# Kernel optimization log

Measured on AMD Instinct MI355X. Metric: run time of the kernel, lower is better.

## Reference

```python
import jax, jax.numpy as jnp
import numpy as np

N = 16384       # number of points (single graph; batch all zeros)
DIN = 3         # input_dim
DOUT = 3        # output_dim
H = 16          # hidden_dim
K = 16          # k nearest neighbors
L = 4           # n_edgeconvs


def setup_inputs() -> dict:
    key = jax.random.key(0)
    ks = jax.random.split(key, 6)
    def w(k, shape, fan_in):
        return jax.random.normal(k, shape, jnp.float32) / np.float32(np.sqrt(fan_in))
    return {
        "x":     jax.random.normal(ks[0], (N, DIN), jnp.float32),
        "emb_W": w(ks[1], (DIN, H), DIN),
        "emb_b": jnp.zeros((H,), jnp.float32),
        "ec_W1": w(ks[2], (L, 2 * H, H), 2 * H),
        "ec_b1": jnp.zeros((L, H), jnp.float32),
        "ec_W2": w(ks[3], (L, H, H), H),
        "ec_b2": jnp.zeros((L, H), jnp.float32),
        "out_W": w(ks[4], (L * H, DOUT), L * H),
        "out_b": jnp.zeros((DOUT,), jnp.float32),
    }


def knn_idx(x, k):
    """Indices [N, k] of k nearest neighbors (no self-loops), like torch_cluster.knn_graph."""
    x = jax.lax.stop_gradient(x)  # graph construction is non-differentiable
    sq = jnp.sum(x * x, axis=-1)
    d = sq[:, None] + sq[None, :] - 2.0 * (x @ x.T)  # [N, N] squared distances
    n = x.shape[0]
    d = d.at[jnp.arange(n), jnp.arange(n)].set(jnp.inf)  # exclude self
    _, idx = jax.lax.top_k(-d, k)
    return idx  # idx[i] = k nearest neighbors j of center i


def edgeconv(x, idx, W1, b1, W2, b2):
    """EdgeConv with aggr='mean': mean_j MLP([x_i, x_j - x_i])."""
    nbr = x[idx]                                      # [N, K, H] gather
    ctr = jnp.broadcast_to(x[:, None, :], nbr.shape)  # [N, K, H]
    feat = jnp.concatenate([ctr, nbr - ctr], axis=-1) # [N, K, 2H]
    msg = jax.nn.relu(feat @ W1 + b1) @ W2 + b2       # [N, K, H]
    return jnp.mean(msg, axis=1)                      # exact k-regular scatter-mean


def reference(x, emb_W, emb_b, ec_W1, ec_b1, ec_W2, ec_b2, out_W, out_b):
    h = jax.nn.relu(x @ emb_W + emb_b)  # embedding
    outs = []
    for l in range(L):  # small fixed layer loop
        idx = knn_idx(h, K)  # kNN graph rebuilt on current features each layer
        h = edgeconv(h, idx, ec_W1[l], ec_b1[l], ec_W2[l], ec_b2[l])
        outs.append(h)
    return jnp.concatenate(outs, axis=-1) @ out_W + out_b  # [N, DOUT]
```

## Files before the change

### kernel.cpp

```cpp
#include <hip/hip_runtime.h>
#include <hip/hip_bf16.h>

#define GN 16384
#define GH 16
#define GK 16
#define GL 4
#define HPS 20

#define RPB 32
#define NTHR 1024
#define CAP 160
#define BSTR 161
#define SSTR 264
#define TILE_C 256
#define TILE_F (TILE_C*HPS)
#define LDS_TILE (2*RPB*BSTR + 2*RPB)
#define LDS_TOT  (LDS_TILE + TILE_F)

#define INFF __builtin_inff()

#define OFF_H     0
#define OFF_IDX   (5*GN*HPS)
#define OFF_FLAGS (OFF_IDX + GN*GK)
#define OFF_XF    (OFF_FLAGS + GN)
#define OFF_EMBW  (OFF_XF + GN*3)
#define OFF_EMBB  (OFF_EMBW + 3*GH)
#define OFF_W1    (OFF_EMBB + GH)
#define OFF_B1    (OFF_W1 + GL*2*GH*GH)
#define OFF_B2_   (OFF_B1 + GL*GH)
#define OFF_W2    OFF_B2_
#define OFF_B2    (OFF_W2 + GL*GH*GH)
#define OFF_OW    (OFF_B2 + GL*GH)
#define OFF_OB    (OFF_OW + GL*GH*3)
#define OFF_DFLAG (OFF_OB + 4)

__global__ void detect_kernel(const unsigned short* __restrict__ raw,
                              int* __restrict__ flag)
{
    if (threadIdx.x == 0 && blockIdx.x == 0) {
        int cnt = 0;
        for (int i = 0; i < 64; ++i) {
            unsigned int bits = ((unsigned int)raw[2*i]) << 16;
            float v = __uint_as_float(bits);
            float a = fabsf(v);
            if (a > 1e-4f && a < 50.f) ++cnt;
        }
        *flag = (cnt >= 32) ? 1 : 0;
    }
}

__global__ void convert_kernel(const void* __restrict__ src,
                               float* __restrict__ dst, int n,
                               const int* __restrict__ flag)
{
    int i = blockIdx.x * 256 + threadIdx.x;
    if (i >= n) return;
    if (*flag)
        dst[i] = __bfloat162float(((const __hip_bfloat16*)src)[i]);
    else
        dst[i] = ((const float*)src)[i];
}

__device__ __forceinline__ float distt(const float hi[16], float sqi,
                                       const float* __restrict__ hj)
{
    float4 A = *(const float4*)(hj + 0);
    float4 B = *(const float4*)(hj + 4);
    float4 C = *(const float4*)(hj + 8);
    float4 D = *(const float4*)(hj + 12);
    float sqj = hj[16];
    float d0 = hi[0]*A.x;
    float d1 = hi[1]*A.y;
    d0 = fmaf(hi[2],  A.z, d0);  d1 = fmaf(hi[3],  A.w, d1);
    d0 = fmaf(hi[4],  B.x, d0);  d1 = fmaf(hi[5],  B.y, d1);
    d0 = fmaf(hi[6],  B.z, d0);  d1 = fmaf(hi[7],  B.w, d1);
    d0 = fmaf(hi[8],  C.x, d0);  d1 = fmaf(hi[9],  C.y, d1);
    d0 = fmaf(hi[10], C.z, d0);  d1 = fmaf(hi[11], C.w, d1);
    d0 = fmaf(hi[12], D.x, d0);  d1 = fmaf(hi[13], D.y, d1);
    d0 = fmaf(hi[14], D.z, d0);  d1 = fmaf(hi[15], D.w, d1);
    return fmaf(-2.f, d0 + d1, sqi + sqj);
}

#define LOAD_HI(ptr)                                                        \
    float hi[16]; float sqi;                                                \
    {                                                                       \
        const float* _hr = (ptr);                                           \
        float4 A = *(const float4*)(_hr + 0);                               \
        float4 B = *(const float4*)(_hr + 4);                               \
        float4 C = *(const float4*)(_hr + 8);                               \
        float4 D = *(const float4*)(_hr + 12);                              \
        hi[0]=A.x; hi[1]=A.y; hi[2]=A.z; hi[3]=A.w;                         \
        hi[4]=B.x; hi[5]=B.y; hi[6]=B.z; hi[7]=B.w;                         \
        hi[8]=C.x; hi[9]=C.y; hi[10]=C.z; hi[11]=C.w;                       \
        hi[12]=D.x; hi[13]=D.y; hi[14]=D.z; hi[15]=D.w;                     \
        sqi = _hr[16];                                                      \
    }

__global__ __launch_bounds__(256) void embed_kernel(
    const float* __restrict__ xf, const float* __restrict__ W,
    const float* __restrict__ b, float* __restrict__ h0)
{
    int i = blockIdx.x * 256 + threadIdx.x;
    float x0 = xf[i*3+0], x1 = xf[i*3+1], x2 = xf[i*3+2];
    float* orow = h0 + i * HPS;
    float sq = 0.f;
#pragma unroll
    for (int c = 0; c < GH; ++c) {
        float t = b[c];
        t = fmaf(x0, W[0*GH+c], t);
        t = fmaf(x1, W[1*GH+c], t);
        t = fmaf(x2, W[2*GH+c], t);
        t = fmaxf(t, 0.f);
        orow[c] = t;
        sq = fmaf(t, t, sq);
    }
    orow[16] = sq;
}

__global__ __launch_bounds__(NTHR, 4) void knn3_kernel(
    const float* __restrict__ hp, int* __restrict__ idxout,
    int* __restrict__ flags)
{
    __shared__ float lds[LDS_TOT];
    float*    bufd = lds;
    int*      bufj = (int*)(lds + RPB*BSTR);
    unsigned* cnt  = (unsigned*)(lds + 2*RPB*BSTR);
    float*    tau  = lds + 2*RPB*BSTR + RPB;
    float*    tile = lds + LDS_TILE;

    const int tid  = threadIdx.x;
    const int r    = tid & 31;
    const int slot = tid >> 5;
    const int row  = blockIdx.x * RPB + r;

    LOAD_HI(hp + row * HPS);

#define STAGE(tb, sh)                                                        \
    for (int v = tid; v < TILE_C*5; v += NTHR) {                             \
        int c = v / 5;                                                       \
        int f = v - c*5;                                                     \
        ((float4*)tile)[v] = ((const float4*)hp)[((tb) + (c << (sh)))*5 + f];\
    }

    float t8[8];
#pragma unroll
    for (int s = 0; s < 8; ++s) t8[s] = INFF;
    float mx = INFF; int mxs = 0;
    for (int k = 0; k < GN/1024; ++k) {
        __syncthreads();
        STAGE(k*1024, 2);
        __syncthreads();
        const float* sb = tile + (slot*8)*HPS;
#pragma unroll 2
        for (int t = 0; t < 8; ++t) {
            int j = k*1024 + ((slot*8 + t) << 2);
            float d = distt(hi, sqi, sb + t*HPS);
            if (j == row) d = INFF;
            if (d < mx) {
#pragma unroll
                for (int q = 0; q < 8; ++q) { bool cs = (q == mxs); t8[q] = cs ? d : t8[q]; }
                mx = t8[0]; mxs = 0;
#pragma unroll
                for (int q = 1; q < 8; ++q) { bool cs = (t8[q] >= mx); mx = cs ? t8[q] : mx; mxs = cs ? q : mxs; }
            }
        }
    }
    __syncthreads();
    *(float4*)(lds + r*SSTR + slot*8)     = make_float4(t8[0], t8[1], t8[2], t8[3]);
    *(float4*)(lds + r*SSTR + slot*8 + 4) = make_float4(t8[4], t8[5], t8[6], t8[7]);
    __syncthreads();

    const int mr = tid >> 5, g = tid & 31;
    float s8[8];
    {
        float4 u0 = *(const float4*)(lds + mr*SSTR + g*8);
        float4 u1 = *(const float4*)(lds + mr*SSTR + g*8 + 4);
        s8[0]=u0.x; s8[1]=u0.y; s8[2]=u0.z; s8[3]=u0.w;
        s8[4]=u1.x; s8[5]=u1.y; s8[6]=u1.z; s8[7]=u1.w;
    }
    float tval = INFF;
#pragma unroll
    for (int k = 0; k < 16; ++k) {
        float md = s8[0]; int ms = 0;
#pragma unroll
        for (int q = 1; q < 8; ++q) { bool cs = (s8[q] < md); md = cs ? s8[q] : md; ms = cs ? q : ms; }
        float rv = md; int rl = g;
#pragma unroll
        for (int m = 1; m <= 16; m <<= 1) {
            float ov = __shfl_xor(rv, m, 32);
            int   ol = __shfl_xor(rl, m, 32);
            bool cs = (ov < rv) || (ov == rv && ol < rl);
            rv = cs ? ov : rv; rl = cs ? ol : rl;
        }
        if (rl == g) {
#pragma unroll
            for (int q = 0; q < 8; ++q) if (q == ms) s8[q] = INFF;
        }
        tval = rv;
    }
    if (g == 0) tau[mr] = tval;
    if (tid < RPB) cnt[tid] = 0;
    __syncthreads();

    const float taur = tau[r];
    const int rowoff = r * BSTR;
    for (int k = 0; k < GN/TILE_C; ++k) {
        __syncthreads();
        STAGE(k*TILE_C, 0);
        __syncthreads();
        const float* sb = tile + (slot*8)*HPS;
#pragma unroll 2
        for (int t = 0; t < 8; ++t) {
            int j = k*TILE_C + slot*8 + t;
            float d = distt(hi, sqi, sb + t*HPS);
            if (j == row) d = INFF;
            if (d <= taur) {
                unsigned pos = atomicAdd(&cnt[r], 1u);
                if (pos < CAP) { bufd[rowoff + pos] = d; bufj[rowoff + pos] = j; }
            }
        }
    }
    __syncthreads();

    const unsigned c   = cnt[mr];
    const unsigned lim = c < CAP ? c : CAP;
    float sd[5]; int sj[5];
#pragma unroll
    for (int e = 0; e < 5; ++e) {
        unsigned p = (unsigned)g + 32u*e;
        bool v = p < lim;
        sd[e] = v ? bufd[mr*BSTR + p] : INFF;
        sj[e] = v ? bufj[mr*BSTR + p] : 0x7fffffff;
    }
    const int rowg = blockIdx.x * RPB + mr;
#pragma unroll
    for (int k = 0; k < GK; ++k) {
        float md = sd[0]; int mj = sj[0]; int ms = 0;
#pragma unroll
        for (int e = 1; e < 5; ++e) {
            bool cs = (sd[e] < md) || (sd[e] == md && sj[e] < mj);
            md = cs ? sd[e] : md; mj = cs ? sj[e] : mj; ms = cs ? e : ms;
        }
        float rd = md; int rj = mj;
#pragma unroll
        for (int m = 1; m <= 16; m <<= 1) {
            float od = __shfl_xor(rd, m, 32);
            int   oj = __shfl_xor(rj, m, 32);
            bool cs = (od < rd) || (od == rd && oj < rj);
            rd = cs ? od : rd; rj = cs ? oj : rj;
        }
        if (g == 0) idxout[rowg*GK + k] = rj;
        if (rd == md && rj == mj) {
#pragma unroll
            for (int e = 0; e < 5; ++e) if (e == ms) { sd[e] = INFF; sj[e] = 0x7fffffff; }
        }
    }
    if (g == 0) flags[rowg] = (c > CAP || c < 16u) ? 1 : 0;
#undef STAGE
}

__global__ __launch_bounds__(64) void rescue_kernel(
    const float* __restrict__ hp, const int* __restrict__ flags,
    int* __restrict__ idxout)
{
    const int lane = threadIdx.x;
    const int r0 = blockIdx.x * RPB;
    int f = (lane < RPB) ? flags[r0 + lane] : 0;
    if (__ballot(f != 0) == 0ull) return;
    for (int rr = 0; rr < RPB; ++rr) {
        if (flags[r0 + rr] == 0) continue;
        const int row = r0 + rr;
        LOAD_HI(hp + row * HPS);
        float topd[GK]; int topi[GK];
#pragma unroll
        for (int s = 0; s < GK; ++s) { topd[s] = INFF; topi[s] = -1; }
        float mx = INFF; int mxs = 0;
        for (int s = 0; s < GN/64; ++s) {
            int j = lane + (s << 6);
            float d = distt(hi, sqi, hp + j * HPS);
            if (j == row) d = INFF;
            if (d < mx) {
#pragma unroll
                for (int q = 0; q < GK; ++q) { bool cs = (q == mxs); topd[q] = cs ? d : topd[q]; topi[q] = cs ? j : topi[q]; }
                mx = topd[0]; mxs = 0;
#pragma unroll
                for (int q = 1; q < GK; ++q) { bool cs = (topd[q] >= mx); mx = cs ? topd[q] : mx; mxs = cs ? q : mxs; }
            }
        }
#pragma unroll
        for (int t = 0; t < GK; ++t) {
            float md = topd[0]; int mj = topi[0]; int ms = 0;
#pragma unroll
            for (int q = 1; q < GK; ++q) {
                bool cs = (topd[q] < md) || (topd[q] == md && topi[q] < mj);
                md = cs ? topd[q] : md; mj = cs ? topi[q] : mj; ms = cs ? q : ms;
            }
            float rd = md; int rj = mj;
#pragma unroll
            for (int m = 1; m <= 32; m <<= 1) {
                float od = __shfl_xor(rd, m, 64);
                int   oj = __shfl_xor(rj, m, 64);
                bool cs = (od < rd) || (od == rd && oj < rj);
                rd = cs ? od : rd; rj = cs ? oj : rj;
            }
            if (lane == 0) idxout[row*GK + t] = rj;
            if (rd == md && rj == mj) {
#pragma unroll
                for (int q = 0; q < GK; ++q) if (q == ms) { topd[q] = INFF; topi[q] = 0x7fffffff; }
            }
        }
    }
}

__global__ __launch_bounds__(256) void edgeconv_kernel(
    const float* __restrict__ hin, const int* __restrict__ idx,
    const float* __restrict__ W1, const float* __restrict__ b1,
    const float* __restrict__ W2, const float* __restrict__ b2,
    float* __restrict__ hout)
{
    __shared__ float sW1[2*GH*GH], sW2[GH*GH], sb1[GH], sb2[GH];
    const int tid = threadIdx.x;
    for (int t = tid; t < 2*GH*GH; t += 256) sW1[t] = W1[t];
    for (int t = tid; t < GH*GH;  t += 256) sW2[t] = W2[t];
    if (tid < GH) { sb1[tid] = b1[tid]; sb2[tid] = b2[tid]; }
    __syncthreads();

    const int t4 = tid & 3;
    const int i = blockIdx.x * 64 + (tid >> 2);

    LOAD_HI(hin + i * HPS);
    (void)sqi;
    float ci[GH];
#pragma unroll
    for (int c = 0; c < GH; ++c) {
        float s = sb1[c];
#pragma unroll
        for (int d = 0; d < GH; ++d) s = fmaf(hi[d], sW1[d*GH+c], s);
        ci[c] = s;
    }
    float acc[GH];
#pragma unroll
    for (int c = 0; c < GH; ++c) acc[c] = 0.f;

    const int4 jj = *(const int4*)(idx + i*GK + t4*4);
    const int js[4] = { jj.x, jj.y, jj.z, jj.w };
#pragma unroll
    for (int nn = 0; nn < 4; ++nn) {
        const int j = js[nn];
        float dj[GH];
        {
            const float* hv = hin + j * HPS;
            float4 A = *(const float4*)(hv + 0);
            float4 B = *(const float4*)(hv + 4);
            float4 C = *(const float4*)(hv + 8);
            float4 D = *(const float4*)(hv + 12);
            dj[0]=A.x-hi[0]; dj[1]=A.y-hi[1]; dj[2]=A.z-hi[2]; dj[3]=A.w-hi[3];
            dj[4]=B.x-hi[4]; dj[5]=B.y-hi[5]; dj[6]=B.z-hi[6]; dj[7]=B.w-hi[7];
            dj[8]=C.x-hi[8]; dj[9]=C.y-hi[9]; dj[10]=C.z-hi[10]; dj[11]=C.w-hi[11];
            dj[12]=D.x-hi[12]; dj[13]=D.y-hi[13]; dj[14]=D.z-hi[14]; dj[15]=D.w-hi[15];
        }
        float msg[GH];
#pragma unroll
        for (int c = 0; c < GH; ++c) {
            float s = ci[c];
#pragma unroll
            for (int d = 0; d < GH; ++d) s = fmaf(dj[d], sW1[(GH+d)*GH+c], s);
            msg[c] = fmaxf(s, 0.f);
        }
#pragma unroll
        for (int c2 = 0; c2 < GH; ++c2) {
            float s = acc[c2];
#pragma unroll
            for (int c = 0; c < GH; ++c) s = fmaf(msg[c], sW2[c*GH+c2], s);
            acc[c2] = s;
        }
    }
#pragma unroll
    for (int c = 0; c < GH; ++c) {
        acc[c] += __shfl_xor(acc[c], 1);
        acc[c] += __shfl_xor(acc[c], 2);
    }
    if (t4 == 0) {
        float* orow = hout + i * HPS;
        float sq = 0.f;
#pragma unroll
        for (int c = 0; c < GH; ++c) {
            float v = acc[c] * (1.f/16.f) + sb2[c];
            orow[c] = v;
            sq = fmaf(v, v, sq);
        }
        orow[16] = sq;
    }
}

__global__ __launch_bounds__(256) void out_kernel(
    const float* __restrict__ hbase, const float* __restrict__ W,
    const float* __restrict__ b, void* __restrict__ out,
    const int* __restrict__ flag)
{
    int i = blockIdx.x * 256 + threadIdx.x;
    float a0 = b[0], a1 = b[1], a2 = b[2];
#pragma unroll
    for (int l = 0; l < GL; ++l) {
        const float* hp = hbase + l * GN * HPS + i * HPS;
#pragma unroll
        for (int c = 0; c < GH; ++c) {
            const float v = hp[c];
            const float* wr = W + (l * GH + c) * 3;
            a0 = fmaf(v, wr[0], a0);
            a1 = fmaf(v, wr[1], a1);
            a2 = fmaf(v, wr[2], a2);
        }
    }
    if (*flag) {
        __hip_bfloat16* o = (__hip_bfloat16*)out;
        o[i*3+0] = __float2bfloat16(a0);
        o[i*3+1] = __float2bfloat16(a1);
        o[i*3+2] = __float2bfloat16(a2);
    } else {
        float* o = (float*)out;
        o[i*3+0] = a0; o[i*3+1] = a1; o[i*3+2] = a2;
    }
}

extern "C" void kernel_launch(void* const* d_in, const int* in_sizes, int n_in,
                              void* d_out, int out_size, void* d_ws, size_t ws_size,
                              hipStream_t stream)
{
    float* wsf  = (float*)d_ws;
    int* idxb   = (int*)(wsf + OFF_IDX);
    int* flagsb = (int*)(wsf + OFF_FLAGS);
    int* dflag  = (int*)(wsf + OFF_DFLAG);

    detect_kernel<<<1, 64, 0, stream>>>((const unsigned short*)d_in[0], dflag);

    const int segoff[9] = {OFF_XF, OFF_EMBW, OFF_EMBB, OFF_W1, OFF_B1,
                           OFF_W2, OFF_B2, OFF_OW, OFF_OB};
    const int segn[9]   = {GN*3, 3*GH, GH, GL*2*GH*GH, GL*GH,
                           GL*GH*GH, GL*GH, GL*GH*3, 3};
    for (int s = 0; s < 9; ++s)
        convert_kernel<<<(segn[s] + 255)/256, 256, 0, stream>>>(
            d_in[s], wsf + segoff[s], segn[s], dflag);

    embed_kernel<<<GN/256, 256, 0, stream>>>(
        wsf + OFF_XF, wsf + OFF_EMBW, wsf + OFF_EMBB, wsf + OFF_H);

    for (int l = 0; l < GL; ++l) {
        const float* hin = wsf + OFF_H + l*GN*HPS;
        float* hout      = wsf + OFF_H + (l+1)*GN*HPS;
        knn3_kernel<<<GN/RPB, NTHR, 0, stream>>>(hin, idxb, flagsb);
        rescue_kernel<<<GN/RPB, 64, 0, stream>>>(hin, flagsb, idxb);
        edgeconv_kernel<<<GN/64, 256, 0, stream>>>(hin, idxb,
            wsf + OFF_W1 + l*2*GH*GH, wsf + OFF_B1 + l*GH,
            wsf + OFF_W2 + l*GH*GH,  wsf + OFF_B2 + l*GH, hout);
    }

    out_kernel<<<GN/256, 256, 0, stream>>>(
        wsf + OFF_H + GN*HPS, wsf + OFF_OW, wsf + OFF_OB, d_out, dflag);
}
```

Before: 1.357 ms.

## Register-block kNN over 4 rows per thread with prefetched tiles and top-2 threshold

The kNN kernel now has each thread handle 4 query rows at once, so each staged candidate vector loaded from LDS is reused across 4 distance computations. The first pass keeps a per-thread top-2 (min and second-min) over a 1-in-4 sample instead of a top-8 insertion list, which removes the branchy per-candidate insertion. Global loads for the next tile are software-prefetched into registers before the compute on the current one. The risks are higher register pressure (64 floats of query features per thread at 1024 threads per block) and a possibly looser threshold, which could overflow the candidate buffer and send more rows to the rescue path.

```diff
diff --git a/kernel.cpp b/kernel.cpp
--- a/kernel.cpp
+++ b/kernel.cpp
@@ -27,8 +27,7 @@
 #define OFF_EMBB  (OFF_EMBW + 3*GH)
 #define OFF_W1    (OFF_EMBB + GH)
 #define OFF_B1    (OFF_W1 + GL*2*GH*GH)
-#define OFF_B2_   (OFF_B1 + GL*GH)
-#define OFF_W2    OFF_B2_
+#define OFF_W2    (OFF_B1 + GL*GH)
 #define OFF_B2    (OFF_W2 + GL*GH*GH)
 #define OFF_OW    (OFF_B2 + GL*GH)
 #define OFF_OB    (OFF_OW + GL*GH*3)
@@ -117,7 +116,7 @@
     orow[16] = sq;
 }
 
-__global__ __launch_bounds__(NTHR, 4) void knn3_kernel(
+__global__ __launch_bounds__(NTHR, 4) void knn4_kernel(
     const float* __restrict__ hp, int* __restrict__ idxout,
     int* __restrict__ flags)
 {
@@ -127,47 +126,101 @@
     unsigned* cnt  = (unsigned*)(lds + 2*RPB*BSTR);
     float*    tau  = lds + 2*RPB*BSTR + RPB;
     float*    tile = lds + LDS_TILE;
-
-    const int tid  = threadIdx.x;
-    const int r    = tid & 31;
-    const int slot = tid >> 5;
-    const int row  = blockIdx.x * RPB + r;
-
-    LOAD_HI(hp + row * HPS);
-
-#define STAGE(tb, sh)                                                        \
-    for (int v = tid; v < TILE_C*5; v += NTHR) {                             \
-        int c = v / 5;                                                       \
-        int f = v - c*5;                                                     \
-        ((float4*)tile)[v] = ((const float4*)hp)[((tb) + (c << (sh)))*5 + f];\
-    }
-
-    float t8[8];
-#pragma unroll
-    for (int s = 0; s < 8; ++s) t8[s] = INFF;
-    float mx = INFF; int mxs = 0;
-    for (int k = 0; k < GN/1024; ++k) {
-        __syncthreads();
-        STAGE(k*1024, 2);
-        __syncthreads();
-        const float* sb = tile + (slot*8)*HPS;
-#pragma unroll 2
-        for (int t = 0; t < 8; ++t) {
-            int j = k*1024 + ((slot*8 + t) << 2);
-            float d = distt(hi, sqi, sb + t*HPS);
-            if (j == row) d = INFF;
-            if (d < mx) {
-#pragma unroll
-                for (int q = 0; q < 8; ++q) { bool cs = (q == mxs); t8[q] = cs ? d : t8[q]; }
-                mx = t8[0]; mxs = 0;
-#pragma unroll
-                for (int q = 1; q < 8; ++q) { bool cs = (t8[q] >= mx); mx = cs ? t8[q] : mx; mxs = cs ? q : mxs; }
-            }
-        }
-    }
-    __syncthreads();
-    *(float4*)(lds + r*SSTR + slot*8)     = make_float4(t8[0], t8[1], t8[2], t8[3]);
-    *(float4*)(lds + r*SSTR + slot*8 + 4) = make_float4(t8[4], t8[5], t8[6], t8[7]);
+    float4*   tile4 = (float4*)tile;
+
+    const int tid = threadIdx.x;
+    const int q   = tid & 7;
+    const int s   = tid >> 3;
+    const int r0  = blockIdx.x * RPB + q * 4;
+
+    float hi[4][16]; float sqi[4];
+#pragma unroll
+    for (int rr = 0; rr < 4; ++rr) {
+        const float* hr = hp + (r0 + rr) * HPS;
+        float4 A = *(const float4*)(hr + 0);
+        float4 B = *(const float4*)(hr + 4);
+        float4 C = *(const float4*)(hr + 8);
+        float4 D = *(const float4*)(hr + 12);
+        hi[rr][0]=A.x; hi[rr][1]=A.y; hi[rr][2]=A.z; hi[rr][3]=A.w;
+        hi[rr][4]=B.x; hi[rr][5]=B.y; hi[rr][6]=B.z; hi[rr][7]=B.w;
+        hi[rr][8]=C.x; hi[rr][9]=C.y; hi[rr][10]=C.z; hi[rr][11]=C.w;
+        hi[rr][12]=D.x; hi[rr][13]=D.y; hi[rr][14]=D.z; hi[rr][15]=D.w;
+        sqi[rr] = hr[16];
+    }
+
+    const int c0 = tid / 5, f0 = tid - 5*c0;
+    const bool has2 = tid < (TILE_C*5 - NTHR);
+    const int v1 = tid + NTHR;
+    const int c1 = v1 / 5, f1 = v1 - 5*c1;
+    const float4* hp4 = (const float4*)hp;
+    const int o1a = 20*c0 + f0, o1b = 20*c1 + f1;
+    const int o2a = 5*c0 + f0,  o2b = 5*c1 + f1;
+
+#define DIST4(hjp, jglob, dd)                                               \
+    {                                                                       \
+        const float* _hj = (hjp);                                           \
+        float4 A = *(const float4*)(_hj + 0);                               \
+        float4 B = *(const float4*)(_hj + 4);                               \
+        float4 C = *(const float4*)(_hj + 8);                               \
+        float4 D = *(const float4*)(_hj + 12);                              \
+        float sqj = _hj[16];                                                \
+        _Pragma("unroll")                                                   \
+        for (int rr = 0; rr < 4; ++rr) {                                    \
+            float d0 = hi[rr][0]*A.x;                                       \
+            float d1 = hi[rr][1]*A.y;                                       \
+            d0 = fmaf(hi[rr][2],  A.z, d0);  d1 = fmaf(hi[rr][3],  A.w, d1);\
+            d0 = fmaf(hi[rr][4],  B.x, d0);  d1 = fmaf(hi[rr][5],  B.y, d1);\
+            d0 = fmaf(hi[rr][6],  B.z, d0);  d1 = fmaf(hi[rr][7],  B.w, d1);\
+            d0 = fmaf(hi[rr][8],  C.x, d0);  d1 = fmaf(hi[rr][9],  C.y, d1);\
+            d0 = fmaf(hi[rr][10], C.z, d0);  d1 = fmaf(hi[rr][11], C.w, d1);\
+            d0 = fmaf(hi[rr][12], D.x, d0);  d1 = fmaf(hi[rr][13], D.y, d1);\
+            d0 = fmaf(hi[rr][14], D.z, d0);  d1 = fmaf(hi[rr][15], D.w, d1);\
+            dd[rr] = fmaf(-2.f, d0 + d1, sqi[rr] + sqj);                    \
+        }                                                                   \
+        unsigned u = (unsigned)((jglob) - r0);                              \
+        if (u < 4u) {                                                       \
+            _Pragma("unroll")                                               \
+            for (int rr = 0; rr < 4; ++rr)                                  \
+                if (u == (unsigned)rr) dd[rr] = INFF;                       \
+        }                                                                   \
+    }
+
+    float m1[4], m2[4];
+#pragma unroll
+    for (int rr = 0; rr < 4; ++rr) { m1[rr] = INFF; m2[rr] = INFF; }
+    {
+        float4 ga, gb;
+        ga = hp4[o1a];
+        if (has2) gb = hp4[o1b];
+        for (int k = 0; k < 16; ++k) {
+            __syncthreads();
+            tile4[tid] = ga;
+            if (has2) tile4[v1] = gb;
+            if (k + 1 < 16) {
+                ga = hp4[5120*(k+1) + o1a];
+                if (has2) gb = hp4[5120*(k+1) + o1b];
+            }
+            __syncthreads();
+#pragma unroll
+            for (int cc = 0; cc < 2; ++cc) {
+                const int lc = s + cc*128;
+                const int j = 4*(256*k + lc);
+                float dd[4];
+                DIST4(tile + lc*HPS, j, dd);
+#pragma unroll
+                for (int rr = 0; rr < 4; ++rr) {
+                    float t = fmaxf(m1[rr], dd[rr]);
+                    m1[rr] = fminf(m1[rr], dd[rr]);
+                    m2[rr] = fminf(m2[rr], t);
+                }
+            }
+        }
+    }
+#pragma unroll
+    for (int rr = 0; rr < 4; ++rr) {
+        lds[(q*4+rr)*SSTR + s*2 + 0] = m1[rr];
+        lds[(q*4+rr)*SSTR + s*2 + 1] = m2[rr];
+    }
     __syncthreads();
 
     const int mr = tid >> 5, g = tid & 31;
@@ -183,7 +236,7 @@
     for (int k = 0; k < 16; ++k) {
         float md = s8[0]; int ms = 0;
 #pragma unroll
-        for (int q = 1; q < 8; ++q) { bool cs = (s8[q] < md); md = cs ? s8[q] : md; ms = cs ? q : ms; }
+        for (int e = 1; e < 8; ++e) { bool cs = (s8[e] < md); md = cs ? s8[e] : md; ms = cs ? e : ms; }
         float rv = md; int rl = g;
 #pragma unroll
         for (int m = 1; m <= 16; m <<= 1) {
@@ -194,7 +247,7 @@
         }
         if (rl == g) {
 #pragma unroll
-            for (int q = 0; q < 8; ++q) if (q == ms) s8[q] = INFF;
+            for (int e = 0; e < 8; ++e) if (e == ms) s8[e] = INFF;
         }
         tval = rv;
     }
@@ -202,21 +255,42 @@
     if (tid < RPB) cnt[tid] = 0;
     __syncthreads();
 
-    const float taur = tau[r];
-    const int rowoff = r * BSTR;
-    for (int k = 0; k < GN/TILE_C; ++k) {
-        __syncthreads();
-        STAGE(k*TILE_C, 0);
-        __syncthreads();
-        const float* sb = tile + (slot*8)*HPS;
-#pragma unroll 2
-        for (int t = 0; t < 8; ++t) {
-            int j = k*TILE_C + slot*8 + t;
-            float d = distt(hi, sqi, sb + t*HPS);
-            if (j == row) d = INFF;
-            if (d <= taur) {
-                unsigned pos = atomicAdd(&cnt[r], 1u);
-                if (pos < CAP) { bufd[rowoff + pos] = d; bufj[rowoff + pos] = j; }
+    float tau4[4];
+#pragma unroll
+    for (int rr = 0; rr < 4; ++rr) tau4[rr] = tau[q*4+rr];
+    {
+        float4 ga, gb;
+        ga = hp4[o2a];
+        if (has2) gb = hp4[o2b];
+        for (int k = 0; k < GN/TILE_C; ++k) {
+            __syncthreads();
+            tile4[tid] = ga;
+            if (has2) tile4[v1] = gb;
+            if (k + 1 < GN/TILE_C) {
+                ga = hp4[1280*(k+1) + o2a];
+                if (has2) gb = hp4[1280*(k+1) + o2b];
+            }
+            __syncthreads();
+#pragma unroll
+            for (int cc = 0; cc < 2; ++cc) {
+                const int lc = s + cc*128;
+                const int j = 256*k + lc;
+                float dd[4];
+                DIST4(tile + lc*HPS, j, dd);
+                bool p0 = dd[0] <= tau4[0], p1 = dd[1] <= tau4[1];
+                bool p2 = dd[2] <= tau4[2], p3 = dd[3] <= tau4[3];
+                if (p0 | p1 | p2 | p3) {
+#pragma unroll
+                    for (int rr = 0; rr < 4; ++rr) {
+                        if (dd[rr] <= tau4[rr]) {
+                            unsigned pos = atomicAdd(&cnt[q*4+rr], 1u);
+                            if (pos < CAP) {
+                                bufd[(q*4+rr)*BSTR + pos] = dd[rr];
+                                bufj[(q*4+rr)*BSTR + pos] = j;
+                            }
+                        }
+                    }
+                }
             }
         }
     }
@@ -256,7 +330,7 @@
         }
     }
     if (g == 0) flags[rowg] = (c > CAP || c < 16u) ? 1 : 0;
-#undef STAGE
+#undef DIST4
 }
 
 __global__ __launch_bounds__(64) void rescue_kernel(
@@ -281,19 +355,19 @@
             if (j == row) d = INFF;
             if (d < mx) {
 #pragma unroll
-                for (int q = 0; q < GK; ++q) { bool cs = (q == mxs); topd[q] = cs ? d : topd[q]; topi[q] = cs ? j : topi[q]; }
+                for (int e = 0; e < GK; ++e) { bool cs = (e == mxs); topd[e] = cs ? d : topd[e]; topi[e] = cs ? j : topi[e]; }
                 mx = topd[0]; mxs = 0;
 #pragma unroll
-                for (int q = 1; q < GK; ++q) { bool cs = (topd[q] >= mx); mx = cs ? topd[q] : mx; mxs = cs ? q : mxs; }
+                for (int e = 1; e < GK; ++e) { bool cs = (topd[e] >= mx); mx = cs ? topd[e] : mx; mxs = cs ? e : mxs; }
             }
         }
 #pragma unroll
         for (int t = 0; t < GK; ++t) {
             float md = topd[0]; int mj = topi[0]; int ms = 0;
 #pragma unroll
-            for (int q = 1; q < GK; ++q) {
-                bool cs = (topd[q] < md) || (topd[q] == md && topi[q] < mj);
-                md = cs ? topd[q] : md; mj = cs ? topi[q] : mj; ms = cs ? q : ms;
+            for (int e = 1; e < GK; ++e) {
+                bool cs = (topd[e] < md) || (topd[e] == md && topi[e] < mj);
+                md = cs ? topd[e] : md; mj = cs ? topi[e] : mj; ms = cs ? e : ms;
             }
             float rd = md; int rj = mj;
 #pragma unroll
@@ -306,7 +380,7 @@
             if (lane == 0) idxout[row*GK + t] = rj;
             if (rd == md && rj == mj) {
 #pragma unroll
-                for (int q = 0; q < GK; ++q) if (q == ms) { topd[q] = INFF; topi[q] = 0x7fffffff; }
+                for (int e = 0; e < GK; ++e) if (e == ms) { topd[e] = INFF; topi[e] = 0x7fffffff; }
             }
         }
     }
@@ -448,7 +522,7 @@
     for (int l = 0; l < GL; ++l) {
         const float* hin = wsf + OFF_H + l*GN*HPS;
         float* hout      = wsf + OFF_H + (l+1)*GN*HPS;
-        knn3_kernel<<<GN/RPB, NTHR, 0, stream>>>(hin, idxb, flagsb);
+        knn4_kernel<<<GN/RPB, NTHR, 0, stream>>>(hin, idxb, flagsb);
         rescue_kernel<<<GN/RPB, 64, 0, stream>>>(hin, flagsb, idxb);
         edgeconv_kernel<<<GN/64, 256, 0, stream>>>(hin, idxb,
             wsf + OFF_W1 + l*2*GH*GH, wsf + OFF_B1 + l*GH,
```

After: 1.271 ms. -6.3%, faster.
